# Kernel tuning notes

Hardware: AMD Instinct MI355X
Metric: run time of the kernel (lower is better)

## Reference

```python
import jax, jax.numpy as jnp
import numpy as np

D_MODEL = 1024
N_HEAD = 16
D_K = D_MODEL // N_HEAD
SEQ_LEN = 2048
BATCH = 2
NEG = -1e8


def setup_inputs() -> dict:
    key = jax.random.key(0)
    ks = jax.random.split(key, 8)
    scale = 1.0 / np.sqrt(D_MODEL)
    inp = {
        "input": jax.random.normal(ks[0], (BATCH, SEQ_LEN, D_MODEL), dtype=jnp.float32),
        "mask": jax.random.randint(ks[1], (BATCH, SEQ_LEN), 0, 2) == 1,  # True = masked
        "Wq": jax.random.uniform(ks[2], (D_MODEL, D_MODEL), jnp.float32, -scale, scale),
        "bq": jax.random.uniform(ks[3], (D_MODEL,), jnp.float32, -scale, scale),
        "Wk": jax.random.uniform(ks[4], (D_MODEL, D_MODEL), jnp.float32, -scale, scale),
        "bk": jax.random.uniform(ks[5], (D_MODEL,), jnp.float32, -scale, scale),
        "Wv": jax.random.uniform(ks[6], (D_MODEL, D_MODEL), jnp.float32, -scale, scale),
        "bv": jax.random.uniform(ks[7], (D_MODEL,), jnp.float32, -scale, scale),
    }
    return inp


def reference(input, mask, Wq, bq, Wk, bk, Wv, bv):
    B, S, D = input.shape
    # nn.Linear: y = x @ W^T + b
    def split_heads(x):
        return x.reshape(B, S, N_HEAD, D_K).transpose(0, 2, 1, 3)  # [B,H,S,d_k]

    Q = split_heads(input @ Wq.T + bq)
    K = split_heads(input @ Wk.T + bk)
    V = split_heads(input @ Wv.T + bv)

    scores = jnp.einsum('bhqd,bhkd->bhqk', Q, K) / jnp.sqrt(jnp.float32(D_K))
    # mask [B,S] broadcast over heads and query positions (key mask)
    scores = jnp.where(mask[:, None, None, :], NEG, scores)
    attn = jax.nn.softmax(scores, axis=-1)
    out = jnp.einsum('bhqk,bhkd->bhqd', attn, V)  # [B,H,S,d_k]
    return out.transpose(0, 2, 1, 3).reshape(B, S, D)
```

## Files before the change

### kernel.cpp

```cpp
#include <hip/hip_runtime.h>
#include <hip/hip_bf16.h>
#include <math.h>

#define D_MODEL 1024
#define NH 16
#define DK 64
#define SEQ 2048
#define BATCH 2
#define MTOT (BATCH * SEQ)

typedef unsigned short u16;
typedef unsigned int u32;
typedef short bf16x8 __attribute__((ext_vector_type(8)));
typedef short bf16x4 __attribute__((ext_vector_type(4)));
typedef float f32x4 __attribute__((ext_vector_type(4)));

static constexpr float NEGV2 = -1e8f * 1.44269504089f;
static constexpr float SCL2  = 0.125f * 1.44269504089f;

__device__ __forceinline__ u16 f2bf(float f) {
    union { float f; u32 u; } v; v.f = f;
    u32 r = v.u + 0x7FFFu + ((v.u >> 16) & 1u);
    return (u16)(r >> 16);
}

__device__ __forceinline__ float fexp2(float x) {
#if __has_builtin(__builtin_amdgcn_exp2f)
    return __builtin_amdgcn_exp2f(x);
#else
    return __expf(x * 0.69314718056f);
#endif
}

__device__ __forceinline__ u32 pack2(float lo, float hi) {
    union { __hip_bfloat162 h; u32 u; } cv;
    cv.h = __float22bfloat162_rn(float2{lo, hi});
    return cv.u;
}

__device__ __forceinline__ f32x4 mfma16(bf16x4 a, bf16x4 b, f32x4 c) {
#if __has_builtin(__builtin_amdgcn_mfma_f32_16x16x16_bf16)
    return __builtin_amdgcn_mfma_f32_16x16x16_bf16(a, b, c, 0, 0, 0);
#else
    return __builtin_amdgcn_mfma_f32_16x16x16bf16_1k(a, b, c, 0, 0, 0);
#endif
}

__device__ __forceinline__ void stage16(const u16* g, u16* lds_per_lane) {
#if __has_builtin(__builtin_amdgcn_global_load_lds)
    __builtin_amdgcn_global_load_lds((const __attribute__((address_space(1))) u32*)g,
                                     (__attribute__((address_space(3))) u32*)lds_per_lane,
                                     16, 0, 0);
#else
    *(uint4*)lds_per_lane = *(const uint4*)g;
#endif
}

__global__ __launch_bounds__(256) void convert_bf16(
    const float* __restrict__ X, const float* __restrict__ Wq,
    const float* __restrict__ Wk, const float* __restrict__ Wv,
    u16* __restrict__ Xb, u16* __restrict__ Wb)
{
    const int NX = MTOT * D_MODEL / 4;
    const int NW = D_MODEL * D_MODEL / 4;
    int i = blockIdx.x * 256 + threadIdx.x;
    if (i >= NX + 3 * NW) return;
    float4 v; u16* dst;
    if (i < NX)             { v = ((const float4*)X )[i];            dst = Xb + (size_t)i * 4; }
    else if (i < NX + NW)   { v = ((const float4*)Wq)[i - NX];       dst = Wb + (size_t)(i - NX) * 4; }
    else if (i < NX + 2*NW) { v = ((const float4*)Wk)[i - NX - NW];  dst = Wb + (size_t)NW * 4 + (size_t)(i - NX - NW) * 4; }
    else                    { v = ((const float4*)Wv)[i - NX - 2*NW];dst = Wb + (size_t)NW * 8 + (size_t)(i - NX - 2*NW) * 4; }
    ushort4 o;
    o.x = f2bf(v.x); o.y = f2bf(v.y); o.z = f2bf(v.z); o.w = f2bf(v.w);
    *(ushort4*)dst = o;
}

__global__ __launch_bounds__(256, 2) void proj_mfma(
    const u16* __restrict__ Xb, const u16* __restrict__ Wb,
    const float* __restrict__ bq, const float* __restrict__ bk, const float* __restrict__ bv,
    u16* __restrict__ Qb, u16* __restrict__ Kb, u16* __restrict__ Vb)
{
    __shared__ u16 As[128 * 32];
    __shared__ u16 Bs[128 * 32];

    const int id = blockIdx.x + 32 * blockIdx.y + 256 * blockIdx.z;
    const int swz = (id & 7) * 96 + (id >> 3);
    const int xm = swz & 31;
    const int yn = (swz >> 5) & 7;
    const int zi = swz >> 8;

    const u16* __restrict__ W = Wb + (size_t)zi * D_MODEL * D_MODEL;
    const float* __restrict__ bias = zi == 0 ? bq : (zi == 1 ? bk : bv);
    u16* __restrict__ Out = zi == 0 ? Qb : (zi == 1 ? Kb : Vb);

    const int m0 = xm * 128, n0 = yn * 128;
    const int tid = threadIdx.x, lane = tid & 63, w = tid >> 6;
    const int quad = lane >> 4, l15 = lane & 15;
    const int wr = w >> 1, wc = w & 1;

    f32x4 acc[4][4];
#pragma unroll
    for (int i = 0; i < 4; i++)
#pragma unroll
        for (int j = 0; j < 4; j++) acc[i][j] = (f32x4)0.0f;

    const int srow = 32 * w + (lane >> 2);
    const int scol = (lane & 3) * 8;

    for (int k0 = 0; k0 < D_MODEL; k0 += 32) {
#pragma unroll
        for (int t = 0; t < 2; t++) {
            stage16(Xb + (size_t)(m0 + srow + 16 * t) * D_MODEL + k0 + scol,
                    &As[(32 * w + 16 * t) * 32 + lane * 8]);
            stage16(W + (size_t)(n0 + srow + 16 * t) * D_MODEL + k0 + scol,
                    &Bs[(32 * w + 16 * t) * 32 + lane * 8]);
        }
        __syncthreads();
        bf16x8 af[4], bfr[4];
#pragma unroll
        for (int i = 0; i < 4; i++)
            af[i] = *(const bf16x8*)&As[(wr * 64 + i * 16 + l15) * 32 + quad * 8];
#pragma unroll
        for (int j = 0; j < 4; j++)
            bfr[j] = *(const bf16x8*)&Bs[(wc * 64 + j * 16 + l15) * 32 + quad * 8];
#pragma unroll
        for (int i = 0; i < 4; i++)
#pragma unroll
            for (int j = 0; j < 4; j++)
                acc[i][j] = __builtin_amdgcn_mfma_f32_16x16x32_bf16(af[i], bfr[j], acc[i][j], 0, 0, 0);
        __syncthreads();
    }

    float bj[4];
#pragma unroll
    for (int j = 0; j < 4; j++) bj[j] = bias[n0 + wc * 64 + j * 16 + l15];
#pragma unroll
    for (int i = 0; i < 4; i++) {
#pragma unroll
        for (int j = 0; j < 4; j++) {
#pragma unroll
            for (int r = 0; r < 4; r++) {
                int m = m0 + wr * 64 + i * 16 + quad * 4 + r;
                int n = n0 + wc * 64 + j * 16 + l15;
                int b = m >> 11, s = m & (SEQ - 1);
                int h = n >> 6, d = n & 63;
                Out[(((size_t)b * NH + h) * SEQ + s) * DK + d] = f2bf(acc[i][j][r] + bj[j]);
            }
        }
    }
}

__global__ __launch_bounds__(256, 2) void attn_mfma(
    const u16* __restrict__ Qg, const u16* __restrict__ Kg, const u16* __restrict__ Vg,
    const int* __restrict__ mask, float* __restrict__ out)
{
    constexpr int PADK = 72, PADV = 72;
    __shared__ u16 Ks[2][64 * PADK];
    __shared__ u16 Vt[2][64 * PADV];
    __shared__ float mads[SEQ];

    const int id0 = blockIdx.x + 16 * (blockIdx.y + 16 * blockIdx.z);
    const int nid = (id0 & 7) * 64 + (id0 >> 3);
    const int qt0 = nid & 15, h = (nid >> 4) & 15, b = nid >> 8;

    const int tid = threadIdx.x, lane = tid & 63, w = tid >> 6;
    const int quad = lane >> 4, l15 = lane & 15;
    const size_t bh = (size_t)b * NH + h;
    const u16* __restrict__ Qp = Qg + (bh * SEQ + qt0 * 128) * DK;
    const u16* __restrict__ Kp = Kg + bh * SEQ * DK;
    const u16* __restrict__ Vp = Vg + bh * SEQ * DK;
    const int* __restrict__ mp = mask + b * SEQ;

    for (int i = tid; i < SEQ; i += 256) mads[i] = mp[i] ? NEGV2 : 0.0f;

    const int q0 = w * 32;
    bf16x8 qf[2][2];
#pragma unroll
    for (int qt = 0; qt < 2; qt++)
#pragma unroll
        for (int half = 0; half < 2; half++)
            qf[qt][half] = *(const bf16x8*)(Qp + (size_t)(q0 + qt * 16 + l15) * DK + half * 32 + quad * 8);

    const int skey = tid & 63, sdk = (tid >> 6) * 16;
    const int vkp2 = (tid & 31) * 2, vd0 = (tid >> 5) * 8;

    {
        const u16* kr = Kp + (size_t)skey * DK + sdk;
        bf16x8 k0 = *(const bf16x8*)kr, k1 = *(const bf16x8*)(kr + 8);
        u16* kd = &Ks[0][skey * PADK + sdk];
        *(bf16x8*)kd = k0; *(bf16x8*)(kd + 8) = k1;
        const u16* vr = Vp + (size_t)vkp2 * DK + vd0;
        bf16x8 v0 = *(const bf16x8*)vr, v1 = *(const bf16x8*)(vr + DK);
#pragma unroll
        for (int i = 0; i < 8; i++)
            *(u32*)&Vt[0][(vd0 + i) * PADV + vkp2] = (u32)(u16)v0[i] | ((u32)(u16)v1[i] << 16);
    }
    __syncthreads();

    f32x4 O[4][2];
    f32x4 sacc[2];
#pragma unroll
    for (int dt = 0; dt < 4; dt++)
#pragma unroll
        for (int qt = 0; qt < 2; qt++) O[dt][qt] = (f32x4)0.0f;
    sacc[0] = (f32x4)0.0f; sacc[1] = (f32x4)0.0f;

    for (int kt = 0; kt < SEQ / 64; kt++) {
        const int bb = kt & 1;
        bf16x8 nk0, nk1, nv0, nv1;
        if (kt < SEQ / 64 - 1) {
            const u16* kr = Kp + (size_t)((kt + 1) * 64 + skey) * DK + sdk;
            nk0 = *(const bf16x8*)kr; nk1 = *(const bf16x8*)(kr + 8);
            const u16* vr = Vp + (size_t)((kt + 1) * 64 + vkp2) * DK + vd0;
            nv0 = *(const bf16x8*)vr; nv1 = *(const bf16x8*)(vr + DK);
        }

        f32x4 St[4][2];
#pragma unroll
        for (int ktl = 0; ktl < 4; ktl++) {
            bf16x8 kf0 = *(const bf16x8*)&Ks[bb][(ktl * 16 + l15) * PADK + quad * 8];
            bf16x8 kf1 = *(const bf16x8*)&Ks[bb][(ktl * 16 + l15) * PADK + 32 + quad * 8];
#pragma unroll
            for (int qt = 0; qt < 2; qt++) {
                f32x4 acc = (f32x4)0.0f;
                acc = __builtin_amdgcn_mfma_f32_16x16x32_bf16(kf0, qf[qt][0], acc, 0, 0, 0);
                acc = __builtin_amdgcn_mfma_f32_16x16x32_bf16(kf1, qf[qt][1], acc, 0, 0, 0);
                St[ktl][qt] = acc;
            }
        }

#pragma unroll
        for (int ktl = 0; ktl < 4; ktl++) {
            f32x4 ma = *(const f32x4*)&mads[kt * 64 + ktl * 16 + quad * 4];
#pragma unroll
            for (int qt = 0; qt < 2; qt++)
#pragma unroll
                for (int r = 0; r < 4; r++) {
                    float p = fexp2(St[ktl][qt][r] * SCL2 + ma[r]);
                    St[ktl][qt][r] = p;
                    sacc[qt][r] += p;
                }
        }

        bf16x4 pf[4][2];
#pragma unroll
        for (int ktl = 0; ktl < 4; ktl++)
#pragma unroll
            for (int qt = 0; qt < 2; qt++) {
                union { u32 u[2]; bf16x4 v; } pu;
                pu.u[0] = pack2(St[ktl][qt][0], St[ktl][qt][1]);
                pu.u[1] = pack2(St[ktl][qt][2], St[ktl][qt][3]);
                pf[ktl][qt] = pu.v;
            }

#pragma unroll
        for (int ktl = 0; ktl < 4; ktl++)
#pragma unroll
            for (int dt = 0; dt < 4; dt++) {
                bf16x4 vf = *(const bf16x4*)&Vt[bb][(dt * 16 + l15) * PADV + ktl * 16 + quad * 4];
#pragma unroll
                for (int qt = 0; qt < 2; qt++)
                    O[dt][qt] = mfma16(vf, pf[ktl][qt], O[dt][qt]);
            }

        if (kt < SEQ / 64 - 1) {
            u16* kd = &Ks[bb ^ 1][skey * PADK + sdk];
            *(bf16x8*)kd = nk0; *(bf16x8*)(kd + 8) = nk1;
#pragma unroll
            for (int i = 0; i < 8; i++)
                *(u32*)&Vt[bb ^ 1][(vd0 + i) * PADV + vkp2] = (u32)(u16)nv0[i] | ((u32)(u16)nv1[i] << 16);
        }
        __syncthreads();
    }

    float inv[2];
#pragma unroll
    for (int qt = 0; qt < 2; qt++) {
        float s = (sacc[qt][0] + sacc[qt][1]) + (sacc[qt][2] + sacc[qt][3]);
        s += __shfl_xor(s, 16);
        s += __shfl_xor(s, 32);
        inv[qt] = 1.0f / s;
    }
#pragma unroll
    for (int qt = 0; qt < 2; qt++) {
        int q = qt0 * 128 + q0 + qt * 16 + l15;
        float* op = out + ((size_t)b * SEQ + q) * D_MODEL + h * DK;
#pragma unroll
        for (int dt = 0; dt < 4; dt++)
#pragma unroll
            for (int r = 0; r < 4; r++)
                op[dt * 16 + quad * 4 + r] = O[dt][qt][r] * inv[qt];
    }
}

extern "C" void kernel_launch(void* const* d_in, const int* in_sizes, int n_in,
                              void* d_out, int out_size, void* d_ws, size_t ws_size,
                              hipStream_t stream)
{
    const float* X  = (const float*)d_in[0];
    const int* mask = (const int*)d_in[1];
    const float* Wq = (const float*)d_in[2];
    const float* bq = (const float*)d_in[3];
    const float* Wk = (const float*)d_in[4];
    const float* bk = (const float*)d_in[5];
    const float* Wv = (const float*)d_in[6];
    const float* bv = (const float*)d_in[7];
    float* out = (float*)d_out;

    u16* Xb = (u16*)d_ws;
    u16* Wb = Xb + (size_t)MTOT * D_MODEL;
    u16* Qb = Wb + (size_t)3 * D_MODEL * D_MODEL;
    u16* Kb = Qb + (size_t)BATCH * NH * SEQ * DK;
    u16* Vb = Kb + (size_t)BATCH * NH * SEQ * DK;

    const int ncvt = (MTOT * D_MODEL + 3 * D_MODEL * D_MODEL) / 4;
    convert_bf16<<<(ncvt + 255) / 256, 256, 0, stream>>>(X, Wq, Wk, Wv, Xb, Wb);
    proj_mfma<<<dim3(MTOT / 128, D_MODEL / 128, 3), 256, 0, stream>>>(Xb, Wb, bq, bk, bv, Qb, Kb, Vb);
    attn_mfma<<<dim3(SEQ / 128, NH, BATCH), 256, 0, stream>>>(Qb, Kb, Vb, mask, out);
}
```

Before: 176.2 us.

## Split attention over two key halves and combine with a normalization pass

The attention kernel now splits the key sequence into two halves, doubling the grid to 1024 blocks, and writes unnormalized partial outputs and row sums to workspace. A new combine kernel adds the two halves and divides by the summed denominators. The mask-to-additive-bias conversion moves into the convert kernel, which removes the shared-memory mask buffer and allows the occupancy hint to rise to 4 blocks. This targets low occupancy and poor parallelism on a 256-CU device, at the cost of an extra 32MB fp32 partial-output write and read plus one more launch.

```diff
diff --git a/kernel.cpp b/kernel.cpp
--- a/kernel.cpp
+++ b/kernel.cpp
@@ -59,12 +59,23 @@
 __global__ __launch_bounds__(256) void convert_bf16(
     const float* __restrict__ X, const float* __restrict__ Wq,
     const float* __restrict__ Wk, const float* __restrict__ Wv,
-    u16* __restrict__ Xb, u16* __restrict__ Wb)
+    const int* __restrict__ mask,
+    u16* __restrict__ Xb, u16* __restrict__ Wb, float* __restrict__ madsg)
 {
     const int NX = MTOT * D_MODEL / 4;
     const int NW = D_MODEL * D_MODEL / 4;
+    const int NM = MTOT / 4;
     int i = blockIdx.x * 256 + threadIdx.x;
-    if (i >= NX + 3 * NW) return;
+    if (i >= NX + 3 * NW + NM) return;
+    if (i >= NX + 3 * NW) {
+        int j = i - NX - 3 * NW;
+        int4 mi = ((const int4*)mask)[j];
+        float4 o;
+        o.x = mi.x ? NEGV2 : 0.0f; o.y = mi.y ? NEGV2 : 0.0f;
+        o.z = mi.z ? NEGV2 : 0.0f; o.w = mi.w ? NEGV2 : 0.0f;
+        ((float4*)madsg)[j] = o;
+        return;
+    }
     float4 v; u16* dst;
     if (i < NX)             { v = ((const float4*)X )[i];            dst = Xb + (size_t)i * 4; }
     else if (i < NX + NW)   { v = ((const float4*)Wq)[i - NX];       dst = Wb + (size_t)(i - NX) * 4; }
@@ -150,28 +161,28 @@
     }
 }
 
-__global__ __launch_bounds__(256, 2) void attn_mfma(
+__global__ __launch_bounds__(256, 4) void attn_mfma(
     const u16* __restrict__ Qg, const u16* __restrict__ Kg, const u16* __restrict__ Vg,
-    const int* __restrict__ mask, float* __restrict__ out)
+    const float* __restrict__ madsg, float* __restrict__ Pbuf, float* __restrict__ Lbuf)
 {
     constexpr int PADK = 72, PADV = 72;
+    constexpr int HK = SEQ / 2;
+    constexpr int NT = HK / 64;
     __shared__ u16 Ks[2][64 * PADK];
     __shared__ u16 Vt[2][64 * PADV];
-    __shared__ float mads[SEQ];
-
-    const int id0 = blockIdx.x + 16 * (blockIdx.y + 16 * blockIdx.z);
-    const int nid = (id0 & 7) * 64 + (id0 >> 3);
-    const int qt0 = nid & 15, h = (nid >> 4) & 15, b = nid >> 8;
+
+    const int id0 = blockIdx.x;
+    const int nid = (id0 & 7) * 128 + (id0 >> 3);
+    const int grp = nid & 1;
+    const int qt0 = (nid >> 1) & 15, h = (nid >> 5) & 15, b = nid >> 9;
 
     const int tid = threadIdx.x, lane = tid & 63, w = tid >> 6;
     const int quad = lane >> 4, l15 = lane & 15;
     const size_t bh = (size_t)b * NH + h;
     const u16* __restrict__ Qp = Qg + (bh * SEQ + qt0 * 128) * DK;
-    const u16* __restrict__ Kp = Kg + bh * SEQ * DK;
-    const u16* __restrict__ Vp = Vg + bh * SEQ * DK;
-    const int* __restrict__ mp = mask + b * SEQ;
-
-    for (int i = tid; i < SEQ; i += 256) mads[i] = mp[i] ? NEGV2 : 0.0f;
+    const u16* __restrict__ Kp = Kg + (bh * SEQ + (size_t)grp * HK) * DK;
+    const u16* __restrict__ Vp = Vg + (bh * SEQ + (size_t)grp * HK) * DK;
+    const float* __restrict__ mp = madsg + b * SEQ + grp * HK;
 
     const int q0 = w * 32;
     bf16x8 qf[2][2];
@@ -205,10 +216,10 @@
         for (int qt = 0; qt < 2; qt++) O[dt][qt] = (f32x4)0.0f;
     sacc[0] = (f32x4)0.0f; sacc[1] = (f32x4)0.0f;
 
-    for (int kt = 0; kt < SEQ / 64; kt++) {
+    for (int kt = 0; kt < NT; kt++) {
         const int bb = kt & 1;
         bf16x8 nk0, nk1, nv0, nv1;
-        if (kt < SEQ / 64 - 1) {
+        if (kt < NT - 1) {
             const u16* kr = Kp + (size_t)((kt + 1) * 64 + skey) * DK + sdk;
             nk0 = *(const bf16x8*)kr; nk1 = *(const bf16x8*)(kr + 8);
             const u16* vr = Vp + (size_t)((kt + 1) * 64 + vkp2) * DK + vd0;
@@ -231,7 +242,7 @@
 
 #pragma unroll
         for (int ktl = 0; ktl < 4; ktl++) {
-            f32x4 ma = *(const f32x4*)&mads[kt * 64 + ktl * 16 + quad * 4];
+            f32x4 ma = *(const f32x4*)&mp[kt * 64 + ktl * 16 + quad * 4];
 #pragma unroll
             for (int qt = 0; qt < 2; qt++)
 #pragma unroll
@@ -263,7 +274,7 @@
                     O[dt][qt] = mfma16(vf, pf[ktl][qt], O[dt][qt]);
             }
 
-        if (kt < SEQ / 64 - 1) {
+        if (kt < NT - 1) {
             u16* kd = &Ks[bb ^ 1][skey * PADK + sdk];
             *(bf16x8*)kd = nk0; *(bf16x8*)(kd + 8) = nk1;
 #pragma unroll
@@ -273,24 +284,43 @@
         __syncthreads();
     }
 
-    float inv[2];
 #pragma unroll
     for (int qt = 0; qt < 2; qt++) {
-        float s = (sacc[qt][0] + sacc[qt][1]) + (sacc[qt][2] + sacc[qt][3]);
-        s += __shfl_xor(s, 16);
-        s += __shfl_xor(s, 32);
-        inv[qt] = 1.0f / s;
-    }
-#pragma unroll
-    for (int qt = 0; qt < 2; qt++) {
+        float sum = (sacc[qt][0] + sacc[qt][1]) + (sacc[qt][2] + sacc[qt][3]);
+        sum += __shfl_xor(sum, 16);
+        sum += __shfl_xor(sum, 32);
         int q = qt0 * 128 + q0 + qt * 16 + l15;
-        float* op = out + ((size_t)b * SEQ + q) * D_MODEL + h * DK;
+        if (quad == 0)
+            Lbuf[(((size_t)grp * BATCH + b) * NH + h) * SEQ + q] = sum;
+        float* op = Pbuf + (((size_t)grp * BATCH + b) * SEQ + q) * D_MODEL + h * DK;
 #pragma unroll
         for (int dt = 0; dt < 4; dt++)
 #pragma unroll
             for (int r = 0; r < 4; r++)
-                op[dt * 16 + quad * 4 + r] = O[dt][qt][r] * inv[qt];
-    }
+                op[dt * 16 + quad * 4 + r] = O[dt][qt][r];
+    }
+}
+
+__global__ __launch_bounds__(256) void combine_norm(
+    const float* __restrict__ P, const float* __restrict__ L, float* __restrict__ out)
+{
+    const int total = MTOT * D_MODEL / 4;
+    int i = blockIdx.x * 256 + threadIdx.x;
+    if (i >= total) return;
+    int e = i * 4;
+    int b = e >> 21;
+    int s = (e >> 10) & (SEQ - 1);
+    int h = (e & (D_MODEL - 1)) >> 6;
+    size_t li = ((size_t)b * NH + h) * SEQ + s;
+    float inv = 1.0f / (L[li] + L[(size_t)BATCH * NH * SEQ + li]);
+    float4 p0 = ((const float4*)P)[i];
+    float4 p1 = ((const float4*)P)[i + total];
+    float4 o;
+    o.x = (p0.x + p1.x) * inv;
+    o.y = (p0.y + p1.y) * inv;
+    o.z = (p0.z + p1.z) * inv;
+    o.w = (p0.w + p1.w) * inv;
+    ((float4*)out)[i] = o;
 }
 
 extern "C" void kernel_launch(void* const* d_in, const int* in_sizes, int n_in,
@@ -312,9 +342,13 @@
     u16* Qb = Wb + (size_t)3 * D_MODEL * D_MODEL;
     u16* Kb = Qb + (size_t)BATCH * NH * SEQ * DK;
     u16* Vb = Kb + (size_t)BATCH * NH * SEQ * DK;
-
-    const int ncvt = (MTOT * D_MODEL + 3 * D_MODEL * D_MODEL) / 4;
-    convert_bf16<<<(ncvt + 255) / 256, 256, 0, stream>>>(X, Wq, Wk, Wv, Xb, Wb);
+    float* madsg = (float*)(Vb + (size_t)BATCH * NH * SEQ * DK);
+    float* Pbuf = madsg + MTOT;
+    float* Lbuf = Pbuf + (size_t)2 * MTOT * D_MODEL;
+
+    const int ncvt = (MTOT * D_MODEL + 3 * D_MODEL * D_MODEL + MTOT) / 4;
+    convert_bf16<<<(ncvt + 255) / 256, 256, 0, stream>>>(X, Wq, Wk, Wv, mask, Xb, Wb, madsg);
     proj_mfma<<<dim3(MTOT / 128, D_MODEL / 128, 3), 256, 0, stream>>>(Xb, Wb, bq, bk, bv, Qb, Kb, Vb);
-    attn_mfma<<<dim3(SEQ / 128, NH, BATCH), 256, 0, stream>>>(Qb, Kb, Vb, mask, out);
-}
+    attn_mfma<<<dim3(SEQ / 128 * NH * BATCH * 2), 256, 0, stream>>>(Qb, Kb, Vb, madsg, Pbuf, Lbuf);
+    combine_norm<<<(MTOT * D_MODEL / 4 + 255) / 256, 256, 0, stream>>>(Pbuf, Lbuf, out);
+}
```

Measured after the change: 187.2 us. 6.2% more time.
